# Optimization experiments

Measured on AMD Instinct MI355X. Metric: run time of the kernel, lower is better.

Reference implementation:

```python
import jax, jax.numpy as jnp
import numpy as np

B, NPG, HID, HEADS, L = 8, 512, 128, 8, 4
N = B * NPG
E = 16384
EDIM = HID // 4  # edge_dim = hidden_dim // 4 = 32


def _ln(x, g, b):
    m = x.mean(-1, keepdims=True)
    v = ((x - m) ** 2).mean(-1, keepdims=True)
    return (x - m) / jnp.sqrt(v + 1e-5) * g + b


def setup_inputs() -> dict:
    key = jax.random.key(0)
    ks = jax.random.split(key, 24)
    s = 0.05
    epg = E // B
    base = jnp.repeat(jnp.arange(B) * NPG, epg)
    src = base + jax.random.randint(ks[0], (E,), 0, NPG)
    dst = base + jax.random.randint(ks[1], (E,), 0, NPG)
    d = {
        'x': jax.random.randint(ks[2], (N, 1), 0, 100),
        'edge_index': jnp.stack([src, dst]),
        'edge_attr': jax.random.normal(ks[3], (E, 1), jnp.float32),
        'batch': jnp.repeat(jnp.arange(B), NPG),
        'atom_emb': jax.random.normal(ks[4], (100, HID)) * s,
        'edge_w': jax.random.normal(ks[5], (1, EDIM)) * s,
        'edge_b': jnp.zeros((EDIM,)),
        'wq': jax.random.normal(ks[6], (L, HID, HEADS * HID)) * s,
        'bq': jnp.zeros((L, HEADS * HID)),
        'wk': jax.random.normal(ks[7], (L, HID, HEADS * HID)) * s,
        'bk': jnp.zeros((L, HEADS * HID)),
        'wv': jax.random.normal(ks[8], (L, HID, HEADS * HID)) * s,
        'bv': jnp.zeros((L, HEADS * HID)),
        'we': jax.random.normal(ks[9], (L, EDIM, HEADS * HID)) * s,
        'wskip': jax.random.normal(ks[10], (L, HID, HID)) * s,
        'bskip': jnp.zeros((L, HID)),
        'ln_g': jnp.ones((L, HID)),
        'ln_b': jnp.zeros((L, HID)),
        'mha_in_w': jax.random.normal(ks[11], (HID, 3 * HID)) * s,
        'mha_in_b': jnp.zeros((3 * HID,)),
        'mha_out_w': jax.random.normal(ks[12], (HID, HID)) * s,
        'mha_out_b': jnp.zeros((HID,)),
        'w1': jax.random.normal(ks[13], (HID, HID)) * s,
        'b1': jnp.zeros((HID,)),
        'w2': jax.random.normal(ks[14], (HID, HID // 2)) * s,
        'b2': jnp.zeros((HID // 2,)),
        'w3': jax.random.normal(ks[15], (HID // 2, 3)) * s,
        'b3': jnp.zeros((3,)),
    }
    return d


def reference(x, edge_index, edge_attr, batch, atom_emb, edge_w, edge_b,
              wq, bq, wk, bk, wv, bv, we, wskip, bskip, ln_g, ln_b,
              mha_in_w, mha_in_b, mha_out_w, mha_out_b, w1, b1, w2, b2, w3, b3):
    src, dst = edge_index[0], edge_index[1]
    h = atom_emb[x[:, 0]]                       # [N, HID]
    e = edge_attr @ edge_w + edge_b             # [E, EDIM]
    scale = 1.0 / jnp.sqrt(jnp.float32(HID))    # per-head channel dim = HID
    for i in range(L):
        res = h
        q = (h @ wq[i] + bq[i]).reshape(N, HEADS, HID)
        k = (h @ wk[i] + bk[i]).reshape(N, HEADS, HID)
        v = (h @ wv[i] + bv[i]).reshape(N, HEADS, HID)
        ee = (e @ we[i]).reshape(E, HEADS, HID)
        kj = k[src] + ee                        # [E, HEADS, HID]
        vj = v[src] + ee
        logits = jnp.einsum('ehd,ehd->eh', q[dst], kj) * scale
        m = jax.ops.segment_max(logits, dst, num_segments=N)
        a = jnp.exp(logits - m[dst])
        z = jax.ops.segment_sum(a, dst, num_segments=N)
        a = a / (z[dst] + 1e-16)                # edge softmax per target node
        agg = jax.ops.segment_sum(a[:, :, None] * vj, dst, num_segments=N)
        out = agg.mean(axis=1) + h @ wskip[i] + bskip[i]  # concat=False + root skip
        h = jax.nn.gelu(_ln(out + res, ln_g[i], ln_b[i]), approximate=False)
    # equal-size graphs: ragged->padded conversion is a plain reshape, no padding
    p = h.reshape(B, NPG, HID)
    qkv = p @ mha_in_w + mha_in_b               # [B, n, 3*HID]
    hd = HID // HEADS
    q, k, v = [t.reshape(B, NPG, HEADS, hd).transpose(0, 2, 1, 3)
               for t in jnp.split(qkv, 3, axis=-1)]
    att = jax.nn.softmax(jnp.einsum('bhqd,bhkd->bhqk', q, k) / jnp.sqrt(jnp.float32(hd)), axis=-1)
    o = jnp.einsum('bhqk,bhkd->bhqd', att, v).transpose(0, 2, 1, 3).reshape(B, NPG, HID)
    o = (o @ mha_out_w + mha_out_b).reshape(N, HID)
    y = jax.nn.gelu(o @ w1 + b1, approximate=False)
    y = jax.nn.gelu(y @ w2 + b2, approximate=False)
    return y @ w3 + b3                          # [N, 3]
```

## Files before the change

kernel.cpp:

```cpp
#include <hip/hip_runtime.h>
#include <hip/hip_bf16.h>
#include <math.h>

#define NN 4096
#define NE 16384
#define NLAYERS 4

#define WT_STRIDE 442368

typedef __attribute__((ext_vector_type(8))) short bf16x8;
typedef __attribute__((ext_vector_type(4))) float floatx4;

__device__ __forceinline__ float gelu_f(float x) {
  return 0.5f * x * (1.0f + erff(x * 0.70710678118654752440f));
}

__device__ __forceinline__ void bsplit(float a, unsigned short& hi, unsigned short& lo) {
  __hip_bfloat16 h16 = __float2bfloat16(a);
  hi = *(unsigned short*)&h16;
  const float r = a - __bfloat162float(h16);
  __hip_bfloat16 l16 = __float2bfloat16(r);
  lo = *(unsigned short*)&l16;
}

union F16U { float4 v4[4]; float f[16]; };

__global__ void k_init(const int* __restrict__ x, const float* __restrict__ atom_emb,
                       const float* __restrict__ edge_attr, const float* __restrict__ edge_w,
                       const float* __restrict__ edge_b, float* __restrict__ h,
                       float* __restrict__ ef, int* __restrict__ counts,
                       unsigned short* __restrict__ hhi, unsigned short* __restrict__ hlo) {
  const int idx = blockIdx.x * 256 + threadIdx.x;
  const float hv = atom_emb[x[idx >> 7] * 128 + (idx & 127)];
  h[idx] = hv;
  bsplit(hv, hhi[idx], hlo[idx]);
  ef[idx] = edge_attr[idx >> 5] * edge_w[idx & 31] + edge_b[idx & 31];
  if (idx < NN) counts[idx] = 0;
}

__global__ void k_hist(const int* __restrict__ eidx, int* __restrict__ counts) {
  const int e = blockIdx.x * 256 + threadIdx.x;
  if (e < NE) atomicAdd(&counts[eidx[NE + e]], 1);
}

__global__ void k_scan2(const int* __restrict__ counts, int* __restrict__ offs,
                        const int* __restrict__ eidx, int* __restrict__ elist) {
  __shared__ int tmp[1024];
  __shared__ int sheads[4096];
  const int t = threadIdx.x;
  const int c0 = counts[t*4], c1 = counts[t*4+1], c2 = counts[t*4+2], c3 = counts[t*4+3];
  const int s = c0 + c1 + c2 + c3;
  tmp[t] = s; __syncthreads();
  for (int off = 1; off < 1024; off <<= 1) {
    int v = (t >= off) ? tmp[t - off] : 0;
    __syncthreads();
    tmp[t] += v;
    __syncthreads();
  }
  int base = tmp[t] - s;
  offs[t*4]   = base;                sheads[t*4]   = base;
  offs[t*4+1] = base + c0;           sheads[t*4+1] = base + c0;
  offs[t*4+2] = base + c0 + c1;      sheads[t*4+2] = base + c0 + c1;
  offs[t*4+3] = base + c0 + c1 + c2; sheads[t*4+3] = base + c0 + c1 + c2;
  if (t == 1023) offs[NN] = tmp[1023];
  __syncthreads();
  for (int e = t; e < NE; e += 1024) {
    const int p = atomicAdd(&sheads[eidx[NE + e]], 1);
    elist[p] = e;
  }
}

__global__ __launch_bounds__(256) void k_wcvt(
    const float* __restrict__ wq, const float* __restrict__ wk,
    const float* __restrict__ wv, const float* __restrict__ wsk,
    unsigned short* __restrict__ wthi, unsigned short* __restrict__ wtlo) {
  const int z = blockIdx.z;
  const int layer = z >> 2, mat = z & 3;
  int NC; const float* W; int woff;
  if (mat == 0)      { NC = 1024; W = wq  + (size_t)layer * 131072; woff = 0; }
  else if (mat == 1) { NC = 1024; W = wk  + (size_t)layer * 131072; woff = 131072; }
  else if (mat == 2) { NC = 1024; W = wv  + (size_t)layer * 131072; woff = 262144; }
  else               { NC = 128;  W = wsk + (size_t)layer * 16384;  woff = 393216; }
  const int c0 = blockIdx.x * 64;
  if (c0 >= NC) return;
  const int k0 = blockIdx.y * 64;
  __shared__ unsigned short th[64][65], tl[64][65];
  const int t = threadIdx.x;
  for (int i = t; i < 4096; i += 256) {
    const int kk = i >> 6, c = i & 63;
    bsplit(W[(size_t)(k0 + kk) * NC + c0 + c], th[kk][c], tl[kk][c]);
  }
  __syncthreads();
  unsigned short* oh = wthi + (size_t)layer * WT_STRIDE + woff;
  unsigned short* ol = wtlo + (size_t)layer * WT_STRIDE + woff;
  for (int i = t; i < 4096; i += 256) {
    const int n = i >> 6, k = i & 63;
    oh[(size_t)(c0 + n) * 128 + k0 + k] = th[k][n];
    ol[(size_t)(c0 + n) * 128 + k0 + k] = tl[k][n];
  }
}

__global__ __launch_bounds__(256) void k_wqe(
    const float* __restrict__ wq, const float* __restrict__ bq,
    const float* __restrict__ we, unsigned short* __restrict__ wthi,
    unsigned short* __restrict__ wtlo, float* __restrict__ bqe) {
  const int layer = blockIdx.x >> 3, hh = blockIdx.x & 7;
  const float* wq_l = wq + (size_t)layer * 131072;
  const float* we_l = we + (size_t)layer * 32768;
  const float* bq_l = bq + (size_t)layer * 1024;
  __shared__ float wqS[128][132];
  __shared__ float weS[32][132];
  const int t = threadIdx.x;
  for (int i = t; i < 4096; i += 256) {
    const int d = i >> 5, dd4 = (i & 31) << 2;
    *(float4*)&wqS[d][dd4] = *(const float4*)&wq_l[(size_t)d * 1024 + hh * 128 + dd4];
  }
  for (int i = t; i < 1024; i += 256) {
    const int c = i >> 5, dd4 = (i & 31) << 2;
    *(float4*)&weS[c][dd4] = *(const float4*)&we_l[(size_t)c * 1024 + hh * 128 + dd4];
  }
  __syncthreads();
  const int d = t & 127, cg = t >> 7;
  float acc[16];
  #pragma unroll
  for (int cc = 0; cc < 16; cc++) acc[cc] = 0.f;
  for (int dd = 0; dd < 128; dd++) {
    const float a = wqS[d][dd];
    #pragma unroll
    for (int cc = 0; cc < 16; cc++)
      acc[cc] += a * weS[cg * 16 + cc][dd];
  }
  unsigned short* oh = wthi + (size_t)layer * WT_STRIDE + 409600;
  unsigned short* ol = wtlo + (size_t)layer * WT_STRIDE + 409600;
  #pragma unroll
  for (int cc = 0; cc < 16; cc++) {
    const int j = hh * 32 + cg * 16 + cc;
    unsigned short hi, lo;
    bsplit(acc[cc], hi, lo);
    oh[(size_t)j * 128 + d] = hi;
    ol[(size_t)j * 128 + d] = lo;
  }
  if (t < 32) {
    float s = 0.f;
    for (int dd = 0; dd < 128; dd++) s += bq_l[hh * 128 + dd] * weS[t][dd];
    bqe[layer * 256 + hh * 32 + t] = s;
  }
}

__global__ __launch_bounds__(256) void k_mfqkv(
    const unsigned short* __restrict__ hhi, const unsigned short* __restrict__ hlo,
    const unsigned short* __restrict__ wth, const unsigned short* __restrict__ wtl,
    const float* __restrict__ bq, const float* __restrict__ bk,
    const float* __restrict__ bv, const float* __restrict__ bsk,
    const float* __restrict__ bqe_l,
    float* __restrict__ qb, float* __restrict__ kb,
    float* __restrict__ vb, float* __restrict__ skb, float* __restrict__ qeb) {
  const int xb = blockIdx.x;
  int NC; const float* bias; float* C; int woff; int c0;
  if (xb < 16)      { NC = 1024; bias = bq;    C = qb;  woff = 0;      c0 = xb * 64; }
  else if (xb < 32) { NC = 1024; bias = bk;    C = kb;  woff = 131072; c0 = (xb-16) * 64; }
  else if (xb < 48) { NC = 1024; bias = bv;    C = vb;  woff = 262144; c0 = (xb-32) * 64; }
  else if (xb < 50) { NC = 128;  bias = bsk;   C = skb; woff = 393216; c0 = (xb-48) * 64; }
  else              { NC = 256;  bias = bqe_l; C = qeb; woff = 409600; c0 = (xb-50) * 64; }
  __shared__ unsigned short Ah[64][136], Al[64][136], Wh[64][136], Wl[64][136];
  const int t = threadIdx.x;
  const int n0 = blockIdx.y * 64;
  for (int i = t; i < 1024; i += 256) {
    const int r = i >> 4, c8 = (i & 15) << 3;
    *(uint4*)&Ah[r][c8] = *(const uint4*)&hhi[(size_t)(n0 + r) * 128 + c8];
    *(uint4*)&Al[r][c8] = *(const uint4*)&hlo[(size_t)(n0 + r) * 128 + c8];
    *(uint4*)&Wh[r][c8] = *(const uint4*)&wth[woff + (size_t)(c0 + r) * 128 + c8];
    *(uint4*)&Wl[r][c8] = *(const uint4*)&wtl[woff + (size_t)(c0 + r) * 128 + c8];
  }
  __syncthreads();
  const int w = t >> 6, l = t & 63;
  const int quad = l >> 4, lm = l & 15;
  floatx4 acc[4] = {{0.f,0.f,0.f,0.f},{0.f,0.f,0.f,0.f},{0.f,0.f,0.f,0.f},{0.f,0.f,0.f,0.f}};
  #pragma unroll
  for (int kc = 0; kc < 4; kc++) {
    const int ko = kc * 32 + quad * 8;
    const bf16x8 ah = *(const bf16x8*)&Ah[w * 16 + lm][ko];
    const bf16x8 al = *(const bf16x8*)&Al[w * 16 + lm][ko];
    #pragma unroll
    for (int ct = 0; ct < 4; ct++) {
      const bf16x8 bh = *(const bf16x8*)&Wh[ct * 16 + lm][ko];
      const bf16x8 bl = *(const bf16x8*)&Wl[ct * 16 + lm][ko];
      acc[ct] = __builtin_amdgcn_mfma_f32_16x16x32_bf16(ah, bh, acc[ct], 0, 0, 0);
      acc[ct] = __builtin_amdgcn_mfma_f32_16x16x32_bf16(ah, bl, acc[ct], 0, 0, 0);
      acc[ct] = __builtin_amdgcn_mfma_f32_16x16x32_bf16(al, bh, acc[ct], 0, 0, 0);
    }
  }
  #pragma unroll
  for (int ct = 0; ct < 4; ct++) {
    const int col = c0 + ct * 16 + lm;
    const float bb = bias[col];
    #pragma unroll
    for (int r = 0; r < 4; r++) {
      const int row = n0 + w * 16 + quad * 4 + r;
      C[(size_t)row * NC + col] = acc[ct][r] + bb;
    }
  }
}

__global__ __launch_bounds__(256) void k_gemm2(const float* __restrict__ A,
                                               const float* __restrict__ W,
                                               const float* __restrict__ bias,
                                               float* __restrict__ C, int NC, int gelu) {
  __shared__ float As[128][65];
  __shared__ float Ws[128][64];
  const int t = threadIdx.x;
  const int n0 = blockIdx.y * 64, c0 = blockIdx.x * 64;
  for (int i = t; i < 2048; i += 256) {
    const int r = i & 63, k4 = (i >> 6) << 2;
    const float4 a = *(const float4*)&A[(size_t)(n0 + r) * 128 + k4];
    As[k4+0][r] = a.x; As[k4+1][r] = a.y; As[k4+2][r] = a.z; As[k4+3][r] = a.w;
  }
  for (int i = t; i < 2048; i += 256) {
    const int kk = i >> 4, c4 = (i & 15) << 2;
    *(float4*)&Ws[kk][c4] = *(const float4*)&W[(size_t)kk * NC + c0 + c4];
  }
  __syncthreads();
  const int tr = (t >> 4) << 2;
  const int tc = (t & 15) << 2;
  float acc[4][4];
  #pragma unroll
  for (int i = 0; i < 4; i++)
    #pragma unroll
    for (int j = 0; j < 4; j++) acc[i][j] = 0.f;
  #pragma unroll 8
  for (int k = 0; k < 128; k++) {
    const float4 av = *(const float4*)&As[k][tr];
    const float4 wv = *(const float4*)&Ws[k][tc];
    acc[0][0] += av.x*wv.x; acc[0][1] += av.x*wv.y; acc[0][2] += av.x*wv.z; acc[0][3] += av.x*wv.w;
    acc[1][0] += av.y*wv.x; acc[1][1] += av.y*wv.y; acc[1][2] += av.y*wv.z; acc[1][3] += av.y*wv.w;
    acc[2][0] += av.z*wv.x; acc[2][1] += av.z*wv.y; acc[2][2] += av.z*wv.z; acc[2][3] += av.z*wv.w;
    acc[3][0] += av.w*wv.x; acc[3][1] += av.w*wv.y; acc[3][2] += av.w*wv.z; acc[3][3] += av.w*wv.w;
  }
  const float4 bb = *(const float4*)&bias[c0 + tc];
  #pragma unroll
  for (int i = 0; i < 4; i++) {
    float4 v;
    v.x = acc[i][0] + bb.x; v.y = acc[i][1] + bb.y;
    v.z = acc[i][2] + bb.z; v.w = acc[i][3] + bb.w;
    if (gelu) { v.x = gelu_f(v.x); v.y = gelu_f(v.y); v.z = gelu_f(v.z); v.w = gelu_f(v.w); }
    *(float4*)&C[(size_t)(n0 + tr + i) * NC + c0 + tc] = v;
  }
}

__global__ __launch_bounds__(512) void k_edgepost(
    const float* __restrict__ qb, const float* __restrict__ kb,
    const float* __restrict__ vb, const float* __restrict__ qe,
    const float* __restrict__ ef, const int* __restrict__ offs,
    const int* __restrict__ elist, const int* __restrict__ eidx,
    const float* __restrict__ we_l, const float* __restrict__ skb,
    const float* __restrict__ lng, const float* __restrict__ lnb,
    float* __restrict__ h,
    unsigned short* __restrict__ hhi, unsigned short* __restrict__ hlo) {
  __shared__ float Ss[8][256];
  __shared__ float Am[8][128];
  const int t = threadIdx.x;
  const int wid = t >> 6, lane = t & 63;
  const int n0 = (blockIdx.x & 7) * 512 + (blockIdx.x >> 3) * 8;
  const int n = n0 + wid;
  {
    const int hh = lane >> 3, s8 = lane & 7;
    const int d0 = hh * 128 + s8 * 16;
    F16U qv;
    {
      const float4* qp = (const float4*)(qb + (size_t)n * 1024 + d0);
      #pragma unroll
      for (int i = 0; i < 4; i++) qv.v4[i] = qp[i];
    }
    const float4 qe4 = *(const float4*)(qe + (size_t)n * 256 + hh * 32 + s8 * 4);
    float m = -INFINITY, z = 0.f;
    float acc[16];
    #pragma unroll
    for (int i = 0; i < 16; i++) acc[i] = 0.f;
    float sx = 0.f, sy = 0.f, sz = 0.f, sw = 0.f;
    const int e0 = offs[n], e1 = offs[n + 1];
    for (int tt = e0; tt < e1; tt++) {
      const int e = elist[tt];
      const int src = eidx[e];
      F16U kv;
      {
        const float4* kp = (const float4*)(kb + (size_t)src * 1024 + d0);
        #pragma unroll
        for (int i = 0; i < 4; i++) kv.v4[i] = kp[i];
      }
      const float4 ef4 = *(const float4*)(ef + (size_t)e * 32 + s8 * 4);
      float p0 = qe4.x*ef4.x + qe4.y*ef4.y;
      float p1 = qe4.z*ef4.z + qe4.w*ef4.w;
      float p2 = 0.f, p3 = 0.f;
      #pragma unroll
      for (int i = 0; i < 4; i++) {
        p0 += qv.f[i]      * kv.f[i];
        p1 += qv.f[4 + i]  * kv.f[4 + i];
        p2 += qv.f[8 + i]  * kv.f[8 + i];
        p3 += qv.f[12 + i] * kv.f[12 + i];
      }
      float p = (p0 + p1) + (p2 + p3);
      p += __shfl_xor(p, 1);
      p += __shfl_xor(p, 2);
      p += __shfl_xor(p, 4);
      const float logit = p * 0.08838834764831845f;
      if (logit > m + 8.f) {
        const float f = __expf(m - logit);
        z *= f; sx *= f; sy *= f; sz *= f; sw *= f;
        #pragma unroll
        for (int i = 0; i < 16; i++) acc[i] *= f;
        m = logit;
      }
      const float w = __expf(logit - m);
      z += w;
      F16U vv;
      {
        const float4* vp = (const float4*)(vb + (size_t)src * 1024 + d0);
        #pragma unroll
        for (int i = 0; i < 4; i++) vv.v4[i] = vp[i];
      }
      #pragma unroll
      for (int i = 0; i < 16; i++) acc[i] += w * vv.f[i];
      sx += w * ef4.x; sy += w * ef4.y;
      sz += w * ef4.z; sw += w * ef4.w;
    }
    const float inv = 1.f / (z + 1e-16f);
    *(float4*)&Ss[wid][hh * 32 + s8 * 4] =
        make_float4(sx * inv, sy * inv, sz * inv, sw * inv);
    F16U ov;
    #pragma unroll
    for (int i = 0; i < 16; i++) ov.f[i] = acc[i] * inv;
    #pragma unroll
    for (int mask = 8; mask <= 32; mask <<= 1)
      #pragma unroll
      for (int i = 0; i < 16; i++) ov.f[i] += __shfl_xor(ov.f[i], mask);
    if (hh == 0) {
      #pragma unroll
      for (int i = 0; i < 16; i++) ov.f[i] *= 0.125f;
      #pragma unroll
      for (int i = 0; i < 4; i++)
        *(float4*)&Am[wid][s8 * 16 + i * 4] = ov.v4[i];
    }
  }
  __syncthreads();
  {
    const int col = t & 127, grp = t >> 7;
    float acc0 = 0.f, acc1 = 0.f;
    const float* wp = we_l + col;
    #pragma unroll
    for (int hh2 = 0; hh2 < 8; hh2++) {
      #pragma unroll 4
      for (int c = 0; c < 32; c++) {
        const float wv = wp[(size_t)c * 1024 + hh2 * 128];
        const int k = hh2 * 32 + c;
        acc0 += Ss[grp * 2 + 0][k] * wv;
        acc1 += Ss[grp * 2 + 1][k] * wv;
      }
    }
    const int nA = grp * 2, nB = grp * 2 + 1;
    const size_t oA = (size_t)(n0 + nA) * 128 + col;
    const size_t oB = (size_t)(n0 + nB) * 128 + col;
    Am[nA][col] = Am[nA][col] + 0.125f * acc0 + skb[oA] + h[oA];
    Am[nB][col] = Am[nB][col] + 0.125f * acc1 + skb[oB] + h[oB];
  }
  __syncthreads();
  {
    const float v0 = Am[wid][lane], v1 = Am[wid][lane + 64];
    float s = v0 + v1;
    #pragma unroll
    for (int mask = 1; mask <= 32; mask <<= 1) s += __shfl_xor(s, mask);
    const float mean = s * (1.f / 128.f);
    const float d0 = v0 - mean, d1 = v1 - mean;
    float q = d0 * d0 + d1 * d1;
    #pragma unroll
    for (int mask = 1; mask <= 32; mask <<= 1) q += __shfl_xor(q, mask);
    const float rstd = 1.f / sqrtf(q * (1.f / 128.f) + 1e-5f);
    const float y0 = d0 * rstd * lng[lane] + lnb[lane];
    const float y1 = d1 * rstd * lng[lane + 64] + lnb[lane + 64];
    const float r0 = gelu_f(y0);
    const float r1 = gelu_f(y1);
    const size_t o = (size_t)n * 128 + lane;
    h[o] = r0;
    h[o + 64] = r1;
    bsplit(r0, hhi[o], hlo[o]);
    bsplit(r1, hhi[o + 64], hlo[o + 64]);
  }
}

__global__ __launch_bounds__(256) void k_attn2b(const float* __restrict__ qkvm,
                                                float* __restrict__ pm,
                                                float* __restrict__ pz,
                                                float* __restrict__ pacc) {
  __shared__ float ks2[64][16];
  __shared__ float vs2[64][16];
  const int ksp = blockIdx.x, qt = blockIdx.y, bh = blockIdx.z;
  const int b = bh >> 3, hh = bh & 7;
  const int t = threadIdx.x;
  const size_t rbase = (size_t)(b * 512 + ksp * 64);
  {
    const int j = t >> 2, d4 = (t & 3) << 2;
    const size_t ro = (rbase + j) * 384 + hh * 16 + d4;
    *(float4*)&ks2[j][d4] = *(const float4*)&qkvm[ro + 128];
    *(float4*)&vs2[j][d4] = *(const float4*)&qkvm[ro + 256];
  }
  __syncthreads();
  const int qrow = qt * 256 + t;
  const int nq = b * 512 + qrow;
  F16U qv;
  {
    const float4* qp = (const float4*)(qkvm + (size_t)nq * 384 + hh * 16);
    #pragma unroll
    for (int i = 0; i < 4; i++) qv.v4[i] = qp[i];
  }
  float m = -INFINITY, z = 0.f;
  float acc[16];
  #pragma unroll
  for (int i = 0; i < 16; i++) acc[i] = 0.f;
  for (int j = 0; j < 64; j += 2) {
    F16U k0, k1, v0, v1;
    {
      const float4* p0 = (const float4*)ks2[j];
      const float4* p1 = (const float4*)ks2[j + 1];
      const float4* q0 = (const float4*)vs2[j];
      const float4* q1 = (const float4*)vs2[j + 1];
      #pragma unroll
      for (int i = 0; i < 4; i++) {
        k0.v4[i] = p0[i]; k1.v4[i] = p1[i];
        v0.v4[i] = q0[i]; v1.v4[i] = q1[i];
      }
    }
    float a0 = 0.f, a1 = 0.f, a2 = 0.f, a3 = 0.f;
    float b0 = 0.f, b1 = 0.f, b2 = 0.f, b3 = 0.f;
    #pragma unroll
    for (int i = 0; i < 4; i++) {
      a0 += qv.f[i]      * k0.f[i];
      a1 += qv.f[4 + i]  * k0.f[4 + i];
      a2 += qv.f[8 + i]  * k0.f[8 + i];
      a3 += qv.f[12 + i] * k0.f[12 + i];
      b0 += qv.f[i]      * k1.f[i];
      b1 += qv.f[4 + i]  * k1.f[4 + i];
      b2 += qv.f[8 + i]  * k1.f[8 + i];
      b3 += qv.f[12 + i] * k1.f[12 + i];
    }
    const float sa = ((a0 + a1) + (a2 + a3)) * 0.25f;
    const float sb = ((b0 + b1) + (b2 + b3)) * 0.25f;
    const float smax = fmaxf(sa, sb);
    if (smax > m + 8.f) {
      const float f = __expf(m - smax);
      z *= f;
      #pragma unroll
      for (int i = 0; i < 16; i++) acc[i] *= f;
      m = smax;
    }
    const float wa = __expf(sa - m);
    const float wb = __expf(sb - m);
    z += wa + wb;
    #pragma unroll
    for (int i = 0; i < 16; i++)
      acc[i] += wa * v0.f[i] + wb * v1.f[i];
  }
  const int p = (bh * 512 + qrow) * 8 + ksp;
  pm[p] = m; pz[p] = z;
  float4* pp = (float4*)&pacc[(size_t)p * 16];
  F16U ov;
  #pragma unroll
  for (int i = 0; i < 16; i++) ov.f[i] = acc[i];
  #pragma unroll
  for (int i = 0; i < 4; i++) pp[i] = ov.v4[i];
}

__global__ __launch_bounds__(256) void k_tail(
    const float* __restrict__ pm, const float* __restrict__ pz,
    const float* __restrict__ pacc,
    const float* __restrict__ mow, const float* __restrict__ mob,
    const float* __restrict__ w1, const float* __restrict__ b1,
    const float* __restrict__ w2, const float* __restrict__ b2,
    const float* __restrict__ w3, const float* __restrict__ b3,
    float* __restrict__ out) {
  __shared__ float RA[8][128];
  __shared__ float RB[8][128];
  const int t = threadIdx.x;
  const int w = t >> 6, lane = t & 63;
  const int n0 = blockIdx.x * 8;
  const int rA = w * 2, rB = w * 2 + 1;
  #pragma unroll
  for (int rr = 0; rr < 2; rr++) {
    const int n = n0 + w * 2 + rr;
    const int b = n >> 9, qrow = n & 511;
    #pragma unroll
    for (int half = 0; half < 2; half++) {
      const int c = lane + half * 64;
      const int hh = c >> 4, d = c & 15;
      const int base = ((b * 8 + hh) * 512 + qrow) * 8;
      float ms = pm[base];
      #pragma unroll
      for (int s = 1; s < 8; s++) ms = fmaxf(ms, pm[base + s]);
      float z = 0.f, o = 0.f;
      #pragma unroll
      for (int s = 0; s < 8; s++) {
        const float wg = __expf(pm[base + s] - ms);
        z += pz[base + s] * wg;
        o += pacc[(size_t)(base + s) * 16 + d] * wg;
      }
      RA[w * 2 + rr][c] = o / z;
    }
  }
  {
    const int kk = lane >> 5;
    const int c4 = (lane & 31) << 2;
    float a0x=0.f,a0y=0.f,a0z=0.f,a0w=0.f, a1x=0.f,a1y=0.f,a1z=0.f,a1w=0.f;
    #pragma unroll 8
    for (int i = 0; i < 64; i++) {
      const int k = kk + (i << 1);
      const float4 wv = *(const float4*)&mow[(size_t)k * 128 + c4];
      const float r0 = RA[rA][k], r1 = RA[rB][k];
      a0x += r0*wv.x; a0y += r0*wv.y; a0z += r0*wv.z; a0w += r0*wv.w;
      a1x += r1*wv.x; a1y += r1*wv.y; a1z += r1*wv.z; a1w += r1*wv.w;
    }
    a0x += __shfl_xor(a0x, 32); a0y += __shfl_xor(a0y, 32);
    a0z += __shfl_xor(a0z, 32); a0w += __shfl_xor(a0w, 32);
    a1x += __shfl_xor(a1x, 32); a1y += __shfl_xor(a1y, 32);
    a1z += __shfl_xor(a1z, 32); a1w += __shfl_xor(a1w, 32);
    if (lane < 32) {
      RB[rA][c4+0] = a0x + mob[c4+0]; RB[rA][c4+1] = a0y + mob[c4+1];
      RB[rA][c4+2] = a0z + mob[c4+2]; RB[rA][c4+3] = a0w + mob[c4+3];
      RB[rB][c4+0] = a1x + mob[c4+0]; RB[rB][c4+1] = a1y + mob[c4+1];
      RB[rB][c4+2] = a1z + mob[c4+2]; RB[rB][c4+3] = a1w + mob[c4+3];
    }
  }
  {
    const int kk = lane >> 5;
    const int c4 = (lane & 31) << 2;
    float a0x=0.f,a0y=0.f,a0z=0.f,a0w=0.f, a1x=0.f,a1y=0.f,a1z=0.f,a1w=0.f;
    #pragma unroll 8
    for (int i = 0; i < 64; i++) {
      const int k = kk + (i << 1);
      const float4 wv = *(const float4*)&w1[(size_t)k * 128 + c4];
      const float r0 = RB[rA][k], r1 = RB[rB][k];
      a0x += r0*wv.x; a0y += r0*wv.y; a0z += r0*wv.z; a0w += r0*wv.w;
      a1x += r1*wv.x; a1y += r1*wv.y; a1z += r1*wv.z; a1w += r1*wv.w;
    }
    a0x += __shfl_xor(a0x, 32); a0y += __shfl_xor(a0y, 32);
    a0z += __shfl_xor(a0z, 32); a0w += __shfl_xor(a0w, 32);
    a1x += __shfl_xor(a1x, 32); a1y += __shfl_xor(a1y, 32);
    a1z += __shfl_xor(a1z, 32); a1w += __shfl_xor(a1w, 32);
    if (lane < 32) {
      RA[rA][c4+0] = gelu_f(a0x + b1[c4+0]); RA[rA][c4+1] = gelu_f(a0y + b1[c4+1]);
      RA[rA][c4+2] = gelu_f(a0z + b1[c4+2]); RA[rA][c4+3] = gelu_f(a0w + b1[c4+3]);
      RB[rA][c4+0] = 0.f;
      RA[rB][c4+0] = gelu_f(a1x + b1[c4+0]); RA[rB][c4+1] = gelu_f(a1y + b1[c4+1]);
      RA[rB][c4+2] = gelu_f(a1z + b1[c4+2]); RA[rB][c4+3] = gelu_f(a1w + b1[c4+3]);
    }
  }
  {
    const int kk = lane >> 4;
    const int c4 = (lane & 15) << 2;
    float a0x=0.f,a0y=0.f,a0z=0.f,a0w=0.f, a1x=0.f,a1y=0.f,a1z=0.f,a1w=0.f;
    #pragma unroll 8
    for (int i = 0; i < 32; i++) {
      const int k = kk + (i << 2);
      const float4 wv = *(const float4*)&w2[(size_t)k * 64 + c4];
      const float r0 = RA[rA][k], r1 = RA[rB][k];
      a0x += r0*wv.x; a0y += r0*wv.y; a0z += r0*wv.z; a0w += r0*wv.w;
      a1x += r1*wv.x; a1y += r1*wv.y; a1z += r1*wv.z; a1w += r1*wv.w;
    }
    a0x += __shfl_xor(a0x, 16); a0y += __shfl_xor(a0y, 16);
    a0z += __shfl_xor(a0z, 16); a0w += __shfl_xor(a0w, 16);
    a1x += __shfl_xor(a1x, 16); a1y += __shfl_xor(a1y, 16);
    a1z += __shfl_xor(a1z, 16); a1w += __shfl_xor(a1w, 16);
    a0x += __shfl_xor(a0x, 32); a0y += __shfl_xor(a0y, 32);
    a0z += __shfl_xor(a0z, 32); a0w += __shfl_xor(a0w, 32);
    a1x += __shfl_xor(a1x, 32); a1y += __shfl_xor(a1y, 32);
    a1z += __shfl_xor(a1z, 32); a1w += __shfl_xor(a1w, 32);
    if (lane < 16) {
      RB[rA][c4+0] = gelu_f(a0x + b2[c4+0]); RB[rA][c4+1] = gelu_f(a0y + b2[c4+1]);
      RB[rA][c4+2] = gelu_f(a0z + b2[c4+2]); RB[rA][c4+3] = gelu_f(a0w + b2[c4+3]);
      RB[rB][c4+0] = gelu_f(a1x + b2[c4+0]); RB[rB][c4+1] = gelu_f(a1y + b2[c4+1]);
      RB[rB][c4+2] = gelu_f(a1z + b2[c4+2]); RB[rB][c4+3] = gelu_f(a1w + b2[c4+3]);
    }
  }
  if (lane < 3) {
    #pragma unroll
    for (int rr = 0; rr < 2; rr++) {
      const int row = w * 2 + rr;
      float s = b3[lane];
      for (int c = 0; c < 64; c++) s += RB[row][c] * w3[c * 3 + lane];
      out[(size_t)(n0 + row) * 3 + lane] = s;
    }
  }
}

extern "C" void kernel_launch(void* const* d_in, const int* in_sizes, int n_in,
                              void* d_out, int out_size, void* d_ws, size_t ws_size,
                              hipStream_t stream) {
  const int*   x         = (const int*)d_in[0];
  const int*   eidx      = (const int*)d_in[1];
  const float* edge_attr = (const float*)d_in[2];
  const float* atom_emb  = (const float*)d_in[4];
  const float* edge_w    = (const float*)d_in[5];
  const float* edge_b    = (const float*)d_in[6];
  const float* wq        = (const float*)d_in[7];
  const float* bq        = (const float*)d_in[8];
  const float* wk        = (const float*)d_in[9];
  const float* bk        = (const float*)d_in[10];
  const float* wv        = (const float*)d_in[11];
  const float* bv        = (const float*)d_in[12];
  const float* we        = (const float*)d_in[13];
  const float* wskip     = (const float*)d_in[14];
  const float* bskip     = (const float*)d_in[15];
  const float* ln_g      = (const float*)d_in[16];
  const float* ln_b      = (const float*)d_in[17];
  const float* mha_in_w  = (const float*)d_in[18];
  const float* mha_in_b  = (const float*)d_in[19];
  const float* mha_out_w = (const float*)d_in[20];
  const float* mha_out_b = (const float*)d_in[21];
  const float* w1        = (const float*)d_in[22];
  const float* b1        = (const float*)d_in[23];
  const float* w2        = (const float*)d_in[24];
  const float* b2        = (const float*)d_in[25];
  const float* w3        = (const float*)d_in[26];
  const float* b3        = (const float*)d_in[27];

  float* ws   = (float*)d_ws;
  float* h    = ws;
  float* ef   = h + 524288;
  float* qb   = ef + 524288;
  float* kb   = qb + 4194304;
  float* vb   = kb + 4194304;
  float* qe   = vb + 4194304;
  float* big  = qe + 1048576;
  float* skb  = big + 1048576;
  unsigned short* hhi  = (unsigned short*)(big + 1572864);
  unsigned short* hlo  = hhi + 524288;
  unsigned short* wthi = hlo + 524288;
  unsigned short* wtlo = wthi + 1769472;
  float* sbuf = big + 4194304;
  float* qkvm = qb;
  float* pm   = sbuf;
  float* pz   = sbuf + 262144;
  float* pacc = big;
  int* counts = (int*)(sbuf + 1048576);
  int* offs   = counts + 4100;
  int* heads  = offs + 4100;
  int* elist  = heads + 4100;
  float* bqe  = (float*)(elist + 16384);

  k_init<<<2048, 256, 0, stream>>>(x, atom_emb, edge_attr, edge_w, edge_b, h, ef, counts,
                                   hhi, hlo);
  k_hist<<<64, 256, 0, stream>>>(eidx, counts);
  k_scan2<<<1, 1024, 0, stream>>>(counts, offs, eidx, elist);
  k_wcvt<<<dim3(16, 2, 16), 256, 0, stream>>>(wq, wk, wv, wskip, wthi, wtlo);
  k_wqe<<<32, 256, 0, stream>>>(wq, bq, we, wthi, wtlo, bqe);

  for (int i = 0; i < NLAYERS; i++) {
    const float* bq_i  = bq + (size_t)i * 1024;
    const float* bk_i  = bk + (size_t)i * 1024;
    const float* bv_i  = bv + (size_t)i * 1024;
    const float* we_i  = we + (size_t)i * 32768;
    const float* bsk_i = bskip + (size_t)i * 128;
    const float* g_i   = ln_g + (size_t)i * 128;
    const float* b_i   = ln_b + (size_t)i * 128;
    const unsigned short* wth_i = wthi + (size_t)i * WT_STRIDE;
    const unsigned short* wtl_i = wtlo + (size_t)i * WT_STRIDE;

    k_mfqkv<<<dim3(54, 64), 256, 0, stream>>>(hhi, hlo, wth_i, wtl_i,
                                              bq_i, bk_i, bv_i, bsk_i, bqe + i * 256,
                                              qb, kb, vb, skb, qe);
    k_edgepost<<<512, 512, 0, stream>>>(qb, kb, vb, qe, ef, offs, elist, eidx,
                                        we_i, skb, g_i, b_i, h, hhi, hlo);
  }

  k_gemm2<<<dim3(6, 64), 256, 0, stream>>>(h, mha_in_w, mha_in_b, qkvm, 384, 0);
  k_attn2b<<<dim3(8, 2, 64), 256, 0, stream>>>(qkvm, pm, pz, pacc);
  k_tail<<<512, 256, 0, stream>>>(pm, pz, pacc,
                                  mha_out_w, mha_out_b, w1, b1, w2, b2, w3, b3,
                                  (float*)d_out);
}
```

Measured before the change: 478.3 us.

## Prefetch edge indices, co-issue K/V loads, and make edge-attr projection per-warp

The edge aggregation kernel now prefetches the next edge's index and source ahead of the loop body, and loads K and V for the current edge together so the V gather is not serialized behind the softmax math. The projection of the softmax-weighted edge features through we is rewritten so each warp handles its own node with float4 weight loads and a cross-half shuffle reduction. This removes the two block-wide barriers. Blocks shrink from 8 to 4 nodes (1024 blocks of 256 threads) to raise parallelism. Each warp now reads the full we slice itself, so global and cache traffic for weights rises, and register pressure grows from holding K and V at once.

```diff
diff --git a/kernel.cpp b/kernel.cpp
--- a/kernel.cpp
+++ b/kernel.cpp
@@ -247,7 +247,7 @@
   }
 }
 
-__global__ __launch_bounds__(512) void k_edgepost(
+__global__ __launch_bounds__(256) void k_edgepost(
     const float* __restrict__ qb, const float* __restrict__ kb,
     const float* __restrict__ vb, const float* __restrict__ qe,
     const float* __restrict__ ef, const int* __restrict__ offs,
@@ -256,11 +256,11 @@
     const float* __restrict__ lng, const float* __restrict__ lnb,
     float* __restrict__ h,
     unsigned short* __restrict__ hhi, unsigned short* __restrict__ hlo) {
-  __shared__ float Ss[8][256];
-  __shared__ float Am[8][128];
+  __shared__ float Ss[4][256];
+  __shared__ float Am[4][128];
   const int t = threadIdx.x;
   const int wid = t >> 6, lane = t & 63;
-  const int n0 = (blockIdx.x & 7) * 512 + (blockIdx.x >> 3) * 8;
+  const int n0 = (blockIdx.x & 7) * 512 + (blockIdx.x >> 3) * 4;
   const int n = n0 + wid;
   {
     const int hh = lane >> 3, s8 = lane & 7;
@@ -278,16 +278,18 @@
     for (int i = 0; i < 16; i++) acc[i] = 0.f;
     float sx = 0.f, sy = 0.f, sz = 0.f, sw = 0.f;
     const int e0 = offs[n], e1 = offs[n + 1];
+    int ecur = 0, scur = 0;
+    if (e0 < e1) { ecur = elist[e0]; scur = eidx[ecur]; }
     for (int tt = e0; tt < e1; tt++) {
-      const int e = elist[tt];
-      const int src = eidx[e];
-      F16U kv;
+      F16U kv, vv;
       {
-        const float4* kp = (const float4*)(kb + (size_t)src * 1024 + d0);
+        const float4* kp = (const float4*)(kb + (size_t)scur * 1024 + d0);
+        const float4* vp = (const float4*)(vb + (size_t)scur * 1024 + d0);
         #pragma unroll
-        for (int i = 0; i < 4; i++) kv.v4[i] = kp[i];
+        for (int i = 0; i < 4; i++) { kv.v4[i] = kp[i]; vv.v4[i] = vp[i]; }
       }
-      const float4 ef4 = *(const float4*)(ef + (size_t)e * 32 + s8 * 4);
+      const float4 ef4 = *(const float4*)(ef + (size_t)ecur * 32 + s8 * 4);
+      if (tt + 1 < e1) { ecur = elist[tt + 1]; scur = eidx[ecur]; }
       float p0 = qe4.x*ef4.x + qe4.y*ef4.y;
       float p1 = qe4.z*ef4.z + qe4.w*ef4.w;
       float p2 = 0.f, p3 = 0.f;
@@ -312,12 +314,6 @@
       }
       const float w = __expf(logit - m);
       z += w;
-      F16U vv;
-      {
-        const float4* vp = (const float4*)(vb + (size_t)src * 1024 + d0);
-        #pragma unroll
-        for (int i = 0; i < 4; i++) vv.v4[i] = vp[i];
-      }
       #pragma unroll
       for (int i = 0; i < 16; i++) acc[i] += w * vv.f[i];
       sx += w * ef4.x; sy += w * ef4.y;
@@ -341,28 +337,31 @@
         *(float4*)&Am[wid][s8 * 16 + i * 4] = ov.v4[i];
     }
   }
-  __syncthreads();
-  {
-    const int col = t & 127, grp = t >> 7;
-    float acc0 = 0.f, acc1 = 0.f;
-    const float* wp = we_l + col;
-    #pragma unroll
-    for (int hh2 = 0; hh2 < 8; hh2++) {
-      #pragma unroll 4
-      for (int c = 0; c < 32; c++) {
-        const float wv = wp[(size_t)c * 1024 + hh2 * 128];
-        const int k = hh2 * 32 + c;
-        acc0 += Ss[grp * 2 + 0][k] * wv;
-        acc1 += Ss[grp * 2 + 1][k] * wv;
-      }
-    }
-    const int nA = grp * 2, nB = grp * 2 + 1;
-    const size_t oA = (size_t)(n0 + nA) * 128 + col;
-    const size_t oB = (size_t)(n0 + nB) * 128 + col;
-    Am[nA][col] = Am[nA][col] + 0.125f * acc0 + skb[oA] + h[oA];
-    Am[nB][col] = Am[nB][col] + 0.125f * acc1 + skb[oB] + h[oB];
-  }
-  __syncthreads();
+  {
+    const int half = lane >> 5;
+    const int q4 = (lane & 31) << 2;
+    float ax = 0.f, ay = 0.f, az = 0.f, aw = 0.f;
+    #pragma unroll 8
+    for (int i = 0; i < 128; i++) {
+      const int k = half * 128 + i;
+      const float4 wv = *(const float4*)&we_l[(size_t)(k & 31) * 1024 + (k >> 5) * 128 + q4];
+      const float s = Ss[wid][k];
+      ax += s * wv.x; ay += s * wv.y; az += s * wv.z; aw += s * wv.w;
+    }
+    ax += __shfl_xor(ax, 32); ay += __shfl_xor(ay, 32);
+    az += __shfl_xor(az, 32); aw += __shfl_xor(aw, 32);
+    if (lane < 32) {
+      const size_t o = (size_t)n * 128 + q4;
+      const float4 sk4 = *(const float4*)&skb[o];
+      const float4 h4  = *(const float4*)&h[o];
+      float4 am = *(float4*)&Am[wid][q4];
+      am.x += 0.125f * ax + sk4.x + h4.x;
+      am.y += 0.125f * ay + sk4.y + h4.y;
+      am.z += 0.125f * az + sk4.z + h4.z;
+      am.w += 0.125f * aw + sk4.w + h4.w;
+      *(float4*)&Am[wid][q4] = am;
+    }
+  }
   {
     const float v0 = Am[wid][lane], v1 = Am[wid][lane + 64];
     float s = v0 + v1;
@@ -665,8 +664,8 @@
     k_mfqkv<<<dim3(54, 64), 256, 0, stream>>>(hhi, hlo, wth_i, wtl_i,
                                               bq_i, bk_i, bv_i, bsk_i, bqe + i * 256,
                                               qb, kb, vb, skb, qe);
-    k_edgepost<<<512, 512, 0, stream>>>(qb, kb, vb, qe, ef, offs, elist, eidx,
-                                        we_i, skb, g_i, b_i, h, hhi, hlo);
+    k_edgepost<<<1024, 256, 0, stream>>>(qb, kb, vb, qe, ef, offs, elist, eidx,
+                                         we_i, skb, g_i, b_i, h, hhi, hlo);
   }
 
   k_gemm2<<<dim3(6, 64), 256, 0, stream>>>(h, mha_in_w, mha_in_b, qkvm, 384, 0);
```

New measurement: 454.6 us. 1.05x faster.
